# Optimization experiments

Measured on AMD Instinct MI355X. Metric: run time of the kernel, lower is better.

Reference implementation:

```python
import jax, jax.numpy as jnp
import numpy as np

B, K1, N, DIMS = 512, 11, 5, 784  # K1 = K+1 samples per class incl. query
H = 512  # model_size


def _lstm(x_seq, W, U, b):
    """Keras-style LSTM, return_sequences=True.
    x_seq: [B, T, I]; W: [I, 4H]; U: [H, 4H]; b: [4H]. Gate order i,f,g,o.
    """
    units = U.shape[0]
    bsz = x_seq.shape[0]
    # precompute input projections for all timesteps: [T, B, 4H]
    xw = jnp.einsum('bti,ih->tbh', x_seq, W) + b

    def step(carry, xw_t):
        h, c = carry
        z = xw_t + h @ U  # [B, 4H]
        i, f, g, o = jnp.split(z, 4, axis=-1)
        i = jax.nn.sigmoid(i)
        f = jax.nn.sigmoid(f)
        g = jnp.tanh(g)
        o = jax.nn.sigmoid(o)
        c = f * c + i * g
        h = o * jnp.tanh(c)
        return (h, c), h

    init = (jnp.zeros((bsz, units), x_seq.dtype), jnp.zeros((bsz, units), x_seq.dtype))
    _, hs = jax.lax.scan(step, init, xw)  # hs: [T, B, H]
    return jnp.transpose(hs, (1, 0, 2))  # [B, T, H]


def setup_inputs() -> dict:
    key = jax.random.key(0)
    ks = jax.random.split(key, 8)
    return {
        'input_images': jax.random.normal(ks[0], (B, K1, N, DIMS), jnp.float32),
        'input_labels': jax.random.uniform(ks[1], (B, K1, N, N), jnp.float32),
        'W1': jax.random.normal(ks[2], (N + DIMS, 4 * H), jnp.float32) * 0.02,
        'U1': jax.random.normal(ks[3], (H, 4 * H), jnp.float32) * 0.02,
        'b1': jnp.zeros((4 * H,), jnp.float32),
        'W2': jax.random.normal(ks[4], (H, 4 * N), jnp.float32) * 0.02,
        'U2': jax.random.normal(ks[5], (N, 4 * N), jnp.float32) * 0.02,
        'b2': jnp.zeros((4 * N,), jnp.float32),
    }


def reference(input_images, input_labels, W1, U1, b1, W2, U2, b2):
    K = K1 - 1
    support_imgs = input_images[:, :K]               # [B, K, N, D]
    query_imgs = input_images[:, -1].reshape(-1, 1, N, DIMS)  # [B, 1, N, D]
    support_lbls = input_labels[:, :K]               # [B, K, N, N]
    concat_support = jnp.concatenate([support_imgs, support_lbls], axis=-1)
    zero_lbls = jnp.zeros((B, 1, N, N), input_images.dtype)
    concat_query = jnp.concatenate([query_imgs, zero_lbls], axis=-1)
    seq = jnp.concatenate([concat_support, concat_query], axis=1)  # [B, K1, N, N+D]
    seq = seq.reshape(-1, N * K1, N + DIMS)          # [B, T, N+D], T = N*K1
    x = _lstm(seq, W1, U1, b1)                       # [B, T, H]
    out = _lstm(x, W2, U2, b2)                       # [B, T, N]
    return out.reshape(-1, K1, N, N)
```

## Files before the change

### kernel.cpp

```cpp
#include <hip/hip_runtime.h>

typedef __attribute__((ext_vector_type(8))) __bf16 bf16x8;
typedef __attribute__((ext_vector_type(8))) unsigned short ushort8;
typedef __attribute__((ext_vector_type(4))) float f32x4;
typedef __attribute__((ext_vector_type(2))) unsigned long long u64x2;

#define DEVINL __device__ __forceinline__
#define RLX __ATOMIC_RELAXED
#define AGT __HIP_MEMORY_SCOPE_AGENT

constexpr int B_C    = 512;
constexpr int DIMS_C = 784;
constexpr int T_C    = 55;
constexpr int I0_C   = 789;
constexpr int KP_C   = 800;
constexpr int H_C    = 512;
constexpr int G4_C   = 2048;
constexpr int M1_C   = 28160;

constexpr size_t OFF_A    = 0;
constexpr size_t SZ_A     = (size_t)M1_C * KP_C * 2;
constexpr size_t OFF_W1T  = OFF_A + SZ_A;
constexpr size_t SZ_W1T   = (size_t)G4_C * KP_C * 2;
constexpr size_t OFF_U1T  = OFF_W1T + SZ_W1T;
constexpr size_t SZ_U1T   = (size_t)G4_C * H_C * 2;
constexpr size_t OFF_XW1  = OFF_U1T + SZ_U1T;
constexpr size_t SZ_XW1   = (size_t)M1_C * G4_C * 2;
constexpr size_t OFF_H    = OFF_XW1 + SZ_XW1;
constexpr size_t SZ_H     = (size_t)2 * B_C * H_C * 2;
constexpr size_t OFF_XMID = OFF_H + SZ_H;
constexpr size_t SZ_XMID  = (size_t)M1_C * H_C * 4;
constexpr size_t OFF_XW2  = OFF_XMID + SZ_XMID;
constexpr size_t SZ_XW2   = (size_t)M1_C * 20 * 4;
constexpr size_t OFF_W2T  = OFF_XW2 + SZ_XW2;
constexpr size_t SZ_W2T   = (size_t)20 * H_C * 4;
constexpr size_t OFF_CNT  = OFF_W2T + SZ_W2T;

DEVINL unsigned short f2bf(float f) {
  unsigned u = __builtin_bit_cast(unsigned, f);
  u += 0x7fffu + ((u >> 16) & 1u);
  return (unsigned short)(u >> 16);
}
DEVINL float sigm(float x) {
  return __builtin_amdgcn_rcpf(1.f + __builtin_amdgcn_exp2f(-1.4426950408889634f * x));
}
DEVINL float tanh_(float x) {
  return 2.f * __builtin_amdgcn_rcpf(1.f + __builtin_amdgcn_exp2f(-2.8853900817779268f * x)) - 1.f;
}
DEVINL void gl_lds16(const void* g, void* l) {
  __builtin_amdgcn_global_load_lds((const __attribute__((address_space(1))) void*)g,
                                   (__attribute__((address_space(3))) void*)l, 16, 0, 0);
}
DEVINL void gl_lds16_coh(const void* g, void* l) {
  __builtin_amdgcn_global_load_lds((const __attribute__((address_space(1))) void*)g,
                                   (__attribute__((address_space(3))) void*)l, 16, 0, 17);
}


__global__ void pack_a(const float* __restrict__ img, const float* __restrict__ lbl,
                       unsigned short* __restrict__ A) {
  int gid = blockIdx.x * blockDim.x + threadIdx.x;
  constexpr int CPR = KP_C / 8;
  if (gid >= M1_C * CPR) return;
  int r  = gid / CPR;
  int cc = gid - r * CPR;
  int t = r >> 9, b = r & 511;
  int k1 = t / 5, n = t - k1 * 5;
  int c0 = cc * 8;
  ushort8 v;
  if (c0 + 8 <= DIMS_C) {
    const float* p = img + ((size_t)((b * 11 + k1) * 5 + n)) * DIMS_C + c0;
    f32x4 x0 = *(const f32x4*)(p);
    f32x4 x1 = *(const f32x4*)(p + 4);
#pragma unroll
    for (int j = 0; j < 4; ++j) { v[j] = f2bf(x0[j]); v[4 + j] = f2bf(x1[j]); }
  } else {
#pragma unroll
    for (int j = 0; j < 8; ++j) {
      int c = c0 + j;
      float x = 0.f;
      if (c < DIMS_C) x = img[((size_t)((b * 11 + k1) * 5 + n)) * DIMS_C + c];
      else if (c < I0_C && k1 < 10) x = lbl[((size_t)((b * 11 + k1) * 5 + n)) * 5 + (c - DIMS_C)];
      v[j] = f2bf(x);
    }
  }
  *(ushort8*)(A + (size_t)r * KP_C + c0) = v;
}

__global__ void pack_w1t(const float* __restrict__ W1, unsigned short* __restrict__ W1T) {
  int gid = blockIdx.x * blockDim.x + threadIdx.x;
  if (gid >= G4_C * KP_C) return;
  int col = gid / KP_C, k = gid - col * KP_C;
  float x = (k < I0_C) ? W1[(size_t)k * G4_C + col] : 0.f;
  W1T[(size_t)col * KP_C + k] = f2bf(x);
}

__global__ void pack_u1t(const float* __restrict__ U1, unsigned short* __restrict__ U1T) {
  int gid = blockIdx.x * blockDim.x + threadIdx.x;
  if (gid >= G4_C * H_C) return;
  int col = gid / H_C, k = gid - col * H_C;
  U1T[(size_t)col * H_C + k] = f2bf(U1[(size_t)k * G4_C + col]);
}

__global__ void pack_w2t(const float* __restrict__ W2, float* __restrict__ W2T) {
  int gid = blockIdx.x * blockDim.x + threadIdx.x;
  if (gid >= 20 * H_C) return;
  int col = gid / H_C, k = gid - col * H_C;
  W2T[(size_t)col * H_C + k] = W2[(size_t)k * 20 + col];
}

__launch_bounds__(256, 2)
__global__ void gemm1(const unsigned short* __restrict__ A,
                      const unsigned short* __restrict__ Bt,
                      const float* __restrict__ bias,
                      _Float16* __restrict__ C)
{
  __shared__ unsigned short sA[2][128 * 32];
  __shared__ unsigned short sB[2][128 * 32];
  const int tid = threadIdx.x;
  const int w = tid >> 6, l = tid & 63;
  const int lo = l & 15, hi = l >> 4;
  const int wm = w >> 1, wn = w & 1;
  const int bx = blockIdx.x;
  const int by = blockIdx.y;

  const unsigned short* aSrc[2];
  const unsigned short* bSrc[2];
#pragma unroll
  for (int q = 0; q < 2; ++q) {
    int row = w * 32 + q * 16 + (l >> 2);
    int ch = l & 3;
    int sw = (row >> 1) & 3;
    aSrc[q] = A  + (size_t)(by * 128 + row) * KP_C + (ch ^ sw) * 8;
    bSrc[q] = Bt + (size_t)(bx * 128 + row) * KP_C + (ch ^ sw) * 8;
  }
  int aOff[4], bOff[4];
#pragma unroll
  for (int i = 0; i < 4; ++i) {
    int rA = wm * 64 + i * 16 + lo;
    aOff[i] = rA * 32 + ((hi ^ ((rA >> 1) & 3)) * 8);
    int rB = wn * 64 + i * 16 + lo;
    bOff[i] = rB * 32 + ((hi ^ ((rB >> 1) & 3)) * 8);
  }

  f32x4 acc[4][4];
#pragma unroll
  for (int i = 0; i < 4; ++i)
#pragma unroll
    for (int j = 0; j < 4; ++j) acc[i][j] = (f32x4){0.f, 0.f, 0.f, 0.f};

#define G1_STAGE(buf, ks)                                                  \
  {                                                                        \
    _Pragma("unroll")                                                      \
    for (int q = 0; q < 2; ++q) {                                          \
      gl_lds16(aSrc[q] + (ks) * 32, &sA[buf][w * 1024 + q * 512]);         \
      gl_lds16(bSrc[q] + (ks) * 32, &sB[buf][w * 1024 + q * 512]);         \
    }                                                                      \
  }

  G1_STAGE(0, 0);
  asm volatile("s_waitcnt vmcnt(0)" ::: "memory");
  __syncthreads();

  int cur = 0;
#pragma unroll 1
  for (int ks = 0; ks < KP_C / 32; ++ks) {
    if (ks < KP_C / 32 - 1) G1_STAGE(cur ^ 1, ks + 1);
    bf16x8 af[4], bfr[4];
#pragma unroll
    for (int i = 0; i < 4; ++i) {
      af[i]  = *(const bf16x8*)(&sA[cur][0] + aOff[i]);
      bfr[i] = *(const bf16x8*)(&sB[cur][0] + bOff[i]);
    }
#pragma unroll
    for (int mi = 0; mi < 4; ++mi)
#pragma unroll
      for (int ni = 0; ni < 4; ++ni)
        acc[mi][ni] = __builtin_amdgcn_mfma_f32_16x16x32_bf16(af[mi], bfr[ni], acc[mi][ni], 0, 0, 0);
    asm volatile("s_waitcnt vmcnt(0)" ::: "memory");
    __syncthreads();
    cur ^= 1;
  }
#undef G1_STAGE

  const size_t crow0 = (size_t)by * 128 + wm * 64;
  const int ccol0 = bx * 128 + wn * 64;
#pragma unroll
  for (int ni = 0; ni < 4; ++ni) {
    int col = ccol0 + ni * 16 + lo;
    float bv = bias[col];
#pragma unroll
    for (int mi = 0; mi < 4; ++mi) {
#pragma unroll
      for (int j = 0; j < 4; ++j) {
        size_t row = crow0 + mi * 16 + hi * 4 + j;
        C[row * G4_C + col] = (_Float16)(acc[mi][ni][j] + bv);
      }
    }
  }
}

__launch_bounds__(256, 1)
__global__ void lstm1(const _Float16* __restrict__ xw,
                      const unsigned short* __restrict__ U1T,
                      unsigned short* __restrict__ hbuf,
                      float* __restrict__ xmid,
                      unsigned int* __restrict__ cnt)
{
  __shared__ unsigned short sH[32 * 512];
  __shared__ float sG[4 * 32 * 32];

  const int tid = threadIdx.x;
  const int g = tid >> 6;
  const int l = tid & 63;
  const int lo = l & 15, hi = l >> 4;
  const int bg = blockIdx.x >> 4;
  const int cg = blockIdx.x & 15;
  const int brow0 = bg * 32;
  const int ub = cg * 32;

  bf16x8 bu[2][16];
#pragma unroll
  for (int nf = 0; nf < 2; ++nf) {
    const unsigned short* src = U1T + ((size_t)(g * H_C + ub + nf * 16 + lo)) * H_C + hi * 8;
#pragma unroll
    for (int kk = 0; kk < 16; ++kk)
      bu[nf][kk] = *(const bf16x8*)(src + kk * 32);
  }

  const int s0 = lo & 7;
  const int aO0 = lo * 1024;
  const int aO1 = aO0 + 16 * 1024;

  const int half = l >> 5;
  const int u = l & 31;
  const int rbase = g * 8 + half * 4;
  const int uread = u ^ (((g * 2 + half) & 3) << 3);

  f32x4 c_st = (f32x4){0.f, 0.f, 0.f, 0.f};

  const _Float16* xb = xw + (size_t)(brow0 + rbase) * G4_C + ub + u;
  float xwv[4][4];
#pragma unroll
  for (int g2 = 0; g2 < 4; ++g2)
#pragma unroll
    for (int j = 0; j < 4; ++j)
      xwv[g2][j] = (float)xb[(size_t)j * G4_C + g2 * H_C];

#pragma unroll 1
  for (int t = 0; t < T_C; ++t) {
    f32x4 acc[2][2];
#pragma unroll
    for (int mf = 0; mf < 2; ++mf)
#pragma unroll
      for (int nf = 0; nf < 2; ++nf) acc[mf][nf] = (f32x4){0.f, 0.f, 0.f, 0.f};

    if (t > 0) {
      {
        const unsigned* fp = cnt + (size_t)(bg * 16 + (l & 15)) * 16;
        unsigned target = (unsigned)t;
        while (true) {
          unsigned v = __hip_atomic_load(fp, RLX, AGT);
          if (__all(v >= target)) break;
          __builtin_amdgcn_s_sleep(2);
        }
      }
      asm volatile("" ::: "memory");

      const unsigned short* hsrc = hbuf + (size_t)(t & 1) * (B_C * H_C);
#pragma unroll
      for (int p = 0; p < 8; ++p) {
        int row = g * 8 + p;
        gl_lds16_coh(hsrc + (size_t)(brow0 + row) * H_C + ((l ^ p) * 8),
                     sH + row * 512);
      }
      asm volatile("s_waitcnt vmcnt(0)" ::: "memory");
      __syncthreads();

#pragma unroll
      for (int kk = 0; kk < 16; ++kk) {
        int off = (((kk * 4 + hi) ^ s0) << 4);
        bf16x8 a0 = *(const bf16x8*)((const char*)sH + aO0 + off);
        bf16x8 a1 = *(const bf16x8*)((const char*)sH + aO1 + off);
        acc[0][0] = __builtin_amdgcn_mfma_f32_16x16x32_bf16(a0, bu[0][kk], acc[0][0], 0, 0, 0);
        acc[0][1] = __builtin_amdgcn_mfma_f32_16x16x32_bf16(a0, bu[1][kk], acc[0][1], 0, 0, 0);
        acc[1][0] = __builtin_amdgcn_mfma_f32_16x16x32_bf16(a1, bu[0][kk], acc[1][0], 0, 0, 0);
        acc[1][1] = __builtin_amdgcn_mfma_f32_16x16x32_bf16(a1, bu[1][kk], acc[1][1], 0, 0, 0);
      }
    }

#pragma unroll
    for (int mf = 0; mf < 2; ++mf)
#pragma unroll
      for (int nf = 0; nf < 2; ++nf)
#pragma unroll
        for (int j = 0; j < 4; ++j) {
          int row = mf * 16 + hi * 4 + j;
          sG[g * 1024 + row * 32 + ((nf * 16 + lo) ^ (hi << 3))] = acc[mf][nf][j];
        }
    __syncthreads();

    float hnew[4];
#pragma unroll
    for (int j = 0; j < 4; ++j) {
      int row = rbase + j;
      float zi = sG[0 * 1024 + row * 32 + uread] + xwv[0][j];
      float zf = sG[1 * 1024 + row * 32 + uread] + xwv[1][j];
      float zg = sG[2 * 1024 + row * 32 + uread] + xwv[2][j];
      float zo = sG[3 * 1024 + row * 32 + uread] + xwv[3][j];
      float iv = sigm(zi), fv = sigm(zf), gv = tanh_(zg), ov = sigm(zo);
      float cv = fv * c_st[j] + iv * gv;
      c_st[j] = cv;
      hnew[j] = ov * tanh_(cv);
    }

    if (t < T_C - 1) {
      unsigned short* hd = hbuf + (size_t)((t & 1) ^ 1) * (B_C * H_C);
#pragma unroll
      for (int j = 0; j < 4; ++j) {
        float other = __shfl_xor(hnew[j], 1);
        if ((u & 1) == 0) {
          unsigned val = (unsigned)f2bf(hnew[j]) | ((unsigned)f2bf(other) << 16);
          __hip_atomic_store((unsigned*)(hd + (size_t)(brow0 + rbase + j) * H_C + ub + u), val,
                             RLX, AGT);
        }
      }

      __syncthreads();
      if (tid == 0)
        __hip_atomic_store(&cnt[(size_t)(bg * 16 + cg) * 16], (unsigned)(t + 1), RLX, AGT);

#pragma unroll
      for (int j = 0; j < 4; ++j)
        __builtin_nontemporal_store(hnew[j],
            &xmid[((size_t)t * B_C + brow0 + rbase + j) * H_C + ub + u]);
      const _Float16* xp = xb + (size_t)(t + 1) * B_C * G4_C;
#pragma unroll
      for (int g2 = 0; g2 < 4; ++g2)
#pragma unroll
        for (int j = 0; j < 4; ++j)
          xwv[g2][j] = (float)xp[(size_t)j * G4_C + g2 * H_C];
    } else {
#pragma unroll
      for (int j = 0; j < 4; ++j)
        __builtin_nontemporal_store(hnew[j],
            &xmid[((size_t)t * B_C + brow0 + rbase + j) * H_C + ub + u]);
    }
  }
}

__global__ void gemm2(const float* __restrict__ X,
                      const float* __restrict__ W2T,
                      const float* __restrict__ b2,
                      float* __restrict__ XW2)
{
  int r = blockIdx.x * blockDim.x + threadIdx.x;
  if (r >= M1_C) return;
  float acc[20];
#pragma unroll
  for (int j = 0; j < 20; ++j) acc[j] = b2[j];
  const float* xr = X + (size_t)r * H_C;
  for (int k = 0; k < H_C; k += 4) {
    f32x4 xv = *(const f32x4*)(xr + k);
#pragma unroll
    for (int j = 0; j < 20; ++j) {
      f32x4 wv = *(const f32x4*)(W2T + (size_t)j * H_C + k);
      acc[j] += xv[0]*wv[0] + xv[1]*wv[1] + xv[2]*wv[2] + xv[3]*wv[3];
    }
  }
  float* op = XW2 + (size_t)r * 20;
#pragma unroll
  for (int j = 0; j < 20; ++j) op[j] = acc[j];
}

__global__ void lstm2(const float* __restrict__ XW2,
                      const float* __restrict__ U2,
                      float* __restrict__ out)
{
  int b = blockIdx.x * blockDim.x + threadIdx.x;
  if (b >= B_C) return;
  float u2[5][20];
#pragma unroll
  for (int k = 0; k < 5; ++k)
#pragma unroll
    for (int j = 0; j < 20; ++j) u2[k][j] = U2[k * 20 + j];
  float h[5] = {0, 0, 0, 0, 0}, c[5] = {0, 0, 0, 0, 0};
  for (int t = 0; t < T_C; ++t) {
    const float* xr = XW2 + ((size_t)t * B_C + b) * 20;
    float z[20];
#pragma unroll
    for (int j = 0; j < 20; ++j) z[j] = xr[j];
#pragma unroll
    for (int k = 0; k < 5; ++k) {
      float hk = h[k];
#pragma unroll
      for (int j = 0; j < 20; ++j) z[j] += hk * u2[k][j];
    }
#pragma unroll
    for (int n = 0; n < 5; ++n) {
      float iv = sigm(z[n]), fv = sigm(z[5 + n]), gv = tanh_(z[10 + n]), ov = sigm(z[15 + n]);
      c[n] = fv * c[n] + iv * gv;
      h[n] = ov * tanh_(c[n]);
    }
    int k1 = t / 5, nn = t - k1 * 5;
    float* op = out + (((size_t)b * 11 + k1) * 5 + nn) * 5;
#pragma unroll
    for (int j = 0; j < 5; ++j) op[j] = h[j];
  }
}

extern "C" void kernel_launch(void* const* d_in, const int* in_sizes, int n_in,
                              void* d_out, int out_size, void* d_ws, size_t ws_size,
                              hipStream_t stream) {
  (void)in_sizes; (void)n_in; (void)out_size; (void)ws_size;
  const float* img = (const float*)d_in[0];
  const float* lbl = (const float*)d_in[1];
  const float* W1  = (const float*)d_in[2];
  const float* U1  = (const float*)d_in[3];
  const float* b1  = (const float*)d_in[4];
  const float* W2  = (const float*)d_in[5];
  const float* U2  = (const float*)d_in[6];
  const float* b2  = (const float*)d_in[7];

  char* ws = (char*)d_ws;
  unsigned short* A    = (unsigned short*)(ws + OFF_A);
  unsigned short* W1T  = (unsigned short*)(ws + OFF_W1T);
  unsigned short* U1T  = (unsigned short*)(ws + OFF_U1T);
  _Float16*       XW1  = (_Float16*)      (ws + OFF_XW1);
  unsigned short* HB   = (unsigned short*)(ws + OFF_H);
  float*          XMID = (float*)         (ws + OFF_XMID);
  float*          XW2  = (float*)         (ws + OFF_XW2);
  float*          W2T  = (float*)         (ws + OFF_W2T);
  unsigned int*   CNT  = (unsigned int*)  (ws + OFF_CNT);

  hipMemsetAsync(CNT, 0, 256 * 64, stream);

  pack_a  <<<(M1_C * (KP_C / 8)) / 256, 256, 0, stream>>>(img, lbl, A);
  pack_w1t<<<(G4_C * KP_C) / 256,      256, 0, stream>>>(W1, W1T);
  pack_u1t<<<(G4_C * H_C) / 256,       256, 0, stream>>>(U1, U1T);
  pack_w2t<<<(20 * H_C + 255) / 256,   256, 0, stream>>>(W2, W2T);

  gemm1<<<dim3(G4_C / 128, M1_C / 128), 256, 0, stream>>>(A, W1T, b1, XW1);
  lstm1<<<256, 256, 0, stream>>>(XW1, U1T, HB, XMID, CNT);
  gemm2<<<(M1_C + 255) / 256, 256, 0, stream>>>(XMID, W2T, b2, XW2);
  lstm2<<<8, 64, 0, stream>>>(XW2, U2, (float*)d_out);
}
```

Baseline: 517.3 us.

## Remap LSTM gate columns to registers, drop LDS gate exchange, swizzle GEMM grid

```diff
diff --git a/kernel.cpp b/kernel.cpp
--- a/kernel.cpp
+++ b/kernel.cpp
@@ -121,8 +121,10 @@
   const int w = tid >> 6, l = tid & 63;
   const int lo = l & 15, hi = l >> 4;
   const int wm = w >> 1, wn = w & 1;
-  const int bx = blockIdx.x;
-  const int by = blockIdx.y;
+  const int id = blockIdx.x;
+  const int swz = (id & 7) * 440 + (id >> 3);
+  const int by = swz >> 4;
+  const int bx = swz & 15;
 
   const unsigned short* aSrc[2];
   const unsigned short* bSrc[2];
@@ -208,21 +210,23 @@
                       unsigned int* __restrict__ cnt)
 {
   __shared__ unsigned short sH[32 * 512];
-  __shared__ float sG[4 * 32 * 32];
 
   const int tid = threadIdx.x;
-  const int g = tid >> 6;
+  const int w = tid >> 6;
   const int l = tid & 63;
   const int lo = l & 15, hi = l >> 4;
+  const int q = lo & 7;
+  const int gsel = lo >> 3;
   const int bg = blockIdx.x >> 4;
   const int cg = blockIdx.x & 15;
   const int brow0 = bg * 32;
   const int ub = cg * 32;
+  const int unit = ub + w * 8 + q;
 
   bf16x8 bu[2][16];
 #pragma unroll
   for (int nf = 0; nf < 2; ++nf) {
-    const unsigned short* src = U1T + ((size_t)(g * H_C + ub + nf * 16 + lo)) * H_C + hi * 8;
+    const unsigned short* src = U1T + ((size_t)((nf * 2 + gsel) * H_C + unit)) * H_C + hi * 8;
 #pragma unroll
     for (int kk = 0; kk < 16; ++kk)
       bu[nf][kk] = *(const bf16x8*)(src + kk * 32);
@@ -232,20 +236,19 @@
   const int aO0 = lo * 1024;
   const int aO1 = aO0 + 16 * 1024;
 
-  const int half = l >> 5;
-  const int u = l & 31;
-  const int rbase = g * 8 + half * 4;
-  const int uread = u ^ (((g * 2 + half) & 3) << 3);
-
-  f32x4 c_st = (f32x4){0.f, 0.f, 0.f, 0.f};
-
-  const _Float16* xb = xw + (size_t)(brow0 + rbase) * G4_C + ub + u;
-  float xwv[4][4];
-#pragma unroll
-  for (int g2 = 0; g2 < 4; ++g2)
-#pragma unroll
-    for (int j = 0; j < 4; ++j)
-      xwv[g2][j] = (float)xb[(size_t)j * G4_C + g2 * H_C];
+  float c_st[8];
+#pragma unroll
+  for (int i = 0; i < 8; ++i) c_st[i] = 0.f;
+
+  const _Float16* xb = xw + (size_t)(brow0 + hi * 4) * G4_C + gsel * H_C + unit;
+  float xwv[2][2][4];
+#pragma unroll
+  for (int nf = 0; nf < 2; ++nf)
+#pragma unroll
+    for (int mf = 0; mf < 2; ++mf)
+#pragma unroll
+      for (int j = 0; j < 4; ++j)
+        xwv[nf][mf][j] = (float)xb[(size_t)(mf * 16 + j) * G4_C + nf * 1024];
 
 #pragma unroll 1
   for (int t = 0; t < T_C; ++t) {
@@ -262,7 +265,7 @@
         while (true) {
           unsigned v = __hip_atomic_load(fp, RLX, AGT);
           if (__all(v >= target)) break;
-          __builtin_amdgcn_s_sleep(2);
+          __builtin_amdgcn_s_sleep(1);
         }
       }
       asm volatile("" ::: "memory");
@@ -270,7 +273,7 @@
       const unsigned short* hsrc = hbuf + (size_t)(t & 1) * (B_C * H_C);
 #pragma unroll
       for (int p = 0; p < 8; ++p) {
-        int row = g * 8 + p;
+        int row = w * 8 + p;
         gl_lds16_coh(hsrc + (size_t)(brow0 + row) * H_C + ((l ^ p) * 8),
                      sH + row * 512);
       }
@@ -289,62 +292,72 @@
       }
     }
 
+    float hnew[8];
 #pragma unroll
     for (int mf = 0; mf < 2; ++mf)
 #pragma unroll
-      for (int nf = 0; nf < 2; ++nf)
-#pragma unroll
-        for (int j = 0; j < 4; ++j) {
-          int row = mf * 16 + hi * 4 + j;
-          sG[g * 1024 + row * 32 + ((nf * 16 + lo) ^ (hi << 3))] = acc[mf][nf][j];
-        }
-    __syncthreads();
-
-    float hnew[4];
-#pragma unroll
-    for (int j = 0; j < 4; ++j) {
-      int row = rbase + j;
-      float zi = sG[0 * 1024 + row * 32 + uread] + xwv[0][j];
-      float zf = sG[1 * 1024 + row * 32 + uread] + xwv[1][j];
-      float zg = sG[2 * 1024 + row * 32 + uread] + xwv[2][j];
-      float zo = sG[3 * 1024 + row * 32 + uread] + xwv[3][j];
-      float iv = sigm(zi), fv = sigm(zf), gv = tanh_(zg), ov = sigm(zo);
-      float cv = fv * c_st[j] + iv * gv;
-      c_st[j] = cv;
-      hnew[j] = ov * tanh_(cv);
-    }
+      for (int j = 0; j < 4; ++j) {
+        float za = acc[mf][0][j] + xwv[0][mf][j];
+        float zb = acc[mf][1][j] + xwv[1][mf][j];
+        float zap = __shfl_xor(za, 8);
+        float zbp = __shfl_xor(zb, 8);
+        float zi = gsel ? zap : za;
+        float zf = gsel ? za : zap;
+        float zg = gsel ? zbp : zb;
+        float zo = gsel ? zb : zbp;
+        float iv = sigm(zi), fv = sigm(zf), gv = tanh_(zg), ov = sigm(zo);
+        int ci = mf * 4 + j;
+        float cv = fv * c_st[ci] + iv * gv;
+        c_st[ci] = cv;
+        hnew[ci] = ov * tanh_(cv);
+      }
 
     if (t < T_C - 1) {
       unsigned short* hd = hbuf + (size_t)((t & 1) ^ 1) * (B_C * H_C);
 #pragma unroll
-      for (int j = 0; j < 4; ++j) {
-        float other = __shfl_xor(hnew[j], 1);
-        if ((u & 1) == 0) {
-          unsigned val = (unsigned)f2bf(hnew[j]) | ((unsigned)f2bf(other) << 16);
-          __hip_atomic_store((unsigned*)(hd + (size_t)(brow0 + rbase + j) * H_C + ub + u), val,
-                             RLX, AGT);
+      for (int mf = 0; mf < 2; ++mf)
+#pragma unroll
+        for (int j = 0; j < 4; ++j) {
+          int ci = mf * 4 + j;
+          float other = __shfl_xor(hnew[ci], 1);
+          if (lo < 8 && (q & 1) == 0) {
+            int row = mf * 16 + hi * 4 + j;
+            unsigned val = (unsigned)f2bf(hnew[ci]) | ((unsigned)f2bf(other) << 16);
+            __hip_atomic_store((unsigned*)(hd + (size_t)(brow0 + row) * H_C + unit), val,
+                               RLX, AGT);
+          }
         }
-      }
-
+
+#pragma unroll
+      for (int mf = 0; mf < 2; ++mf)
+#pragma unroll
+        for (int j = 0; j < 4; ++j)
+          if (lo < 8) {
+            int row = mf * 16 + hi * 4 + j;
+            xmid[((size_t)t * B_C + brow0 + row) * H_C + unit] = hnew[mf * 4 + j];
+          }
+      const _Float16* xp = xb + (size_t)(t + 1) * B_C * G4_C;
+#pragma unroll
+      for (int nf = 0; nf < 2; ++nf)
+#pragma unroll
+        for (int mf = 0; mf < 2; ++mf)
+#pragma unroll
+          for (int j = 0; j < 4; ++j)
+            xwv[nf][mf][j] = (float)xp[(size_t)(mf * 16 + j) * G4_C + nf * 1024];
+
+      asm volatile("s_waitcnt vmcnt(0)" ::: "memory");
       __syncthreads();
       if (tid == 0)
         __hip_atomic_store(&cnt[(size_t)(bg * 16 + cg) * 16], (unsigned)(t + 1), RLX, AGT);
-
-#pragma unroll
-      for (int j = 0; j < 4; ++j)
-        __builtin_nontemporal_store(hnew[j],
-            &xmid[((size_t)t * B_C + brow0 + rbase + j) * H_C + ub + u]);
-      const _Float16* xp = xb + (size_t)(t + 1) * B_C * G4_C;
-#pragma unroll
-      for (int g2 = 0; g2 < 4; ++g2)
+    } else {
+#pragma unroll
+      for (int mf = 0; mf < 2; ++mf)
 #pragma unroll
         for (int j = 0; j < 4; ++j)
-          xwv[g2][j] = (float)xp[(size_t)j * G4_C + g2 * H_C];
-    } else {
-#pragma unroll
-      for (int j = 0; j < 4; ++j)
-        __builtin_nontemporal_store(hnew[j],
-            &xmid[((size_t)t * B_C + brow0 + rbase + j) * H_C + ub + u]);
+          if (lo < 8) {
+            int row = mf * 16 + hi * 4 + j;
+            xmid[((size_t)t * B_C + brow0 + row) * H_C + unit] = hnew[mf * 4 + j];
+          }
     }
   }
 }
@@ -440,7 +453,7 @@
   pack_u1t<<<(G4_C * H_C) / 256,       256, 0, stream>>>(U1, U1T);
   pack_w2t<<<(20 * H_C + 255) / 256,   256, 0, stream>>>(W2, W2T);
 
-  gemm1<<<dim3(G4_C / 128, M1_C / 128), 256, 0, stream>>>(A, W1T, b1, XW1);
+  gemm1<<<3520, 256, 0, stream>>>(A, W1T, b1, XW1);
   lstm1<<<256, 256, 0, stream>>>(XW1, U1T, HB, XMID, CNT);
   gemm2<<<(M1_C + 255) / 256, 256, 0, stream>>>(XMID, W2T, b2, XW2);
   lstm2<<<8, 64, 0, stream>>>(XW2, U2, (float*)d_out);
```

Result: slower. 557.1 us (+7.7%).

## Halve LSTM1 batch rows per block, double grid, and swizzle GEMM1 block order

Applied to the files above, without the earlier changes.

```diff
diff --git a/kernel.cpp b/kernel.cpp
--- a/kernel.cpp
+++ b/kernel.cpp
@@ -121,8 +121,10 @@
   const int w = tid >> 6, l = tid & 63;
   const int lo = l & 15, hi = l >> 4;
   const int wm = w >> 1, wn = w & 1;
-  const int bx = blockIdx.x;
-  const int by = blockIdx.y;
+  const int id = blockIdx.x;
+  const int swz = (id & 7) * 440 + (id >> 3);
+  const int by = swz >> 4;
+  const int bx = swz & 15;
 
   const unsigned short* aSrc[2];
   const unsigned short* bSrc[2];
@@ -200,15 +202,15 @@
   }
 }
 
-__launch_bounds__(256, 1)
+__launch_bounds__(256, 2)
 __global__ void lstm1(const _Float16* __restrict__ xw,
                       const unsigned short* __restrict__ U1T,
                       unsigned short* __restrict__ hbuf,
                       float* __restrict__ xmid,
                       unsigned int* __restrict__ cnt)
 {
-  __shared__ unsigned short sH[32 * 512];
-  __shared__ float sG[4 * 32 * 32];
+  __shared__ unsigned short sH[16 * 512];
+  __shared__ float sG[4 * 16 * 32];
 
   const int tid = threadIdx.x;
   const int g = tid >> 6;
@@ -216,7 +218,7 @@
   const int lo = l & 15, hi = l >> 4;
   const int bg = blockIdx.x >> 4;
   const int cg = blockIdx.x & 15;
-  const int brow0 = bg * 32;
+  const int brow0 = bg * 16;
   const int ub = cg * 32;
 
   bf16x8 bu[2][16];
@@ -230,30 +232,27 @@
 
   const int s0 = lo & 7;
   const int aO0 = lo * 1024;
-  const int aO1 = aO0 + 16 * 1024;
 
   const int half = l >> 5;
   const int u = l & 31;
-  const int rbase = g * 8 + half * 4;
-  const int uread = u ^ (((g * 2 + half) & 3) << 3);
-
-  f32x4 c_st = (f32x4){0.f, 0.f, 0.f, 0.f};
+  const int rbase = g * 4 + half * 2;
+  const int uread = u ^ (g << 3);
+
+  float c_st[2] = {0.f, 0.f};
 
   const _Float16* xb = xw + (size_t)(brow0 + rbase) * G4_C + ub + u;
-  float xwv[4][4];
+  float xwv[4][2];
 #pragma unroll
   for (int g2 = 0; g2 < 4; ++g2)
 #pragma unroll
-    for (int j = 0; j < 4; ++j)
+    for (int j = 0; j < 2; ++j)
       xwv[g2][j] = (float)xb[(size_t)j * G4_C + g2 * H_C];
 
 #pragma unroll 1
   for (int t = 0; t < T_C; ++t) {
-    f32x4 acc[2][2];
-#pragma unroll
-    for (int mf = 0; mf < 2; ++mf)
-#pragma unroll
-      for (int nf = 0; nf < 2; ++nf) acc[mf][nf] = (f32x4){0.f, 0.f, 0.f, 0.f};
+    f32x4 acc[2];
+    acc[0] = (f32x4){0.f, 0.f, 0.f, 0.f};
+    acc[1] = (f32x4){0.f, 0.f, 0.f, 0.f};
 
     if (t > 0) {
       {
@@ -262,16 +261,16 @@
         while (true) {
           unsigned v = __hip_atomic_load(fp, RLX, AGT);
           if (__all(v >= target)) break;
-          __builtin_amdgcn_s_sleep(2);
+          __builtin_amdgcn_s_sleep(1);
         }
       }
       asm volatile("" ::: "memory");
 
       const unsigned short* hsrc = hbuf + (size_t)(t & 1) * (B_C * H_C);
 #pragma unroll
-      for (int p = 0; p < 8; ++p) {
-        int row = g * 8 + p;
-        gl_lds16_coh(hsrc + (size_t)(brow0 + row) * H_C + ((l ^ p) * 8),
+      for (int p = 0; p < 4; ++p) {
+        int row = g * 4 + p;
+        gl_lds16_coh(hsrc + (size_t)(brow0 + row) * H_C + ((l ^ (row & 7)) * 8),
                      sH + row * 512);
       }
       asm volatile("s_waitcnt vmcnt(0)" ::: "memory");
@@ -281,33 +280,28 @@
       for (int kk = 0; kk < 16; ++kk) {
         int off = (((kk * 4 + hi) ^ s0) << 4);
         bf16x8 a0 = *(const bf16x8*)((const char*)sH + aO0 + off);
-        bf16x8 a1 = *(const bf16x8*)((const char*)sH + aO1 + off);
-        acc[0][0] = __builtin_amdgcn_mfma_f32_16x16x32_bf16(a0, bu[0][kk], acc[0][0], 0, 0, 0);
-        acc[0][1] = __builtin_amdgcn_mfma_f32_16x16x32_bf16(a0, bu[1][kk], acc[0][1], 0, 0, 0);
-        acc[1][0] = __builtin_amdgcn_mfma_f32_16x16x32_bf16(a1, bu[0][kk], acc[1][0], 0, 0, 0);
-        acc[1][1] = __builtin_amdgcn_mfma_f32_16x16x32_bf16(a1, bu[1][kk], acc[1][1], 0, 0, 0);
-      }
-    }
-
-#pragma unroll
-    for (int mf = 0; mf < 2; ++mf)
-#pragma unroll
-      for (int nf = 0; nf < 2; ++nf)
-#pragma unroll
-        for (int j = 0; j < 4; ++j) {
-          int row = mf * 16 + hi * 4 + j;
-          sG[g * 1024 + row * 32 + ((nf * 16 + lo) ^ (hi << 3))] = acc[mf][nf][j];
-        }
+        acc[0] = __builtin_amdgcn_mfma_f32_16x16x32_bf16(a0, bu[0][kk], acc[0], 0, 0, 0);
+        acc[1] = __builtin_amdgcn_mfma_f32_16x16x32_bf16(a0, bu[1][kk], acc[1], 0, 0, 0);
+      }
+    }
+
+#pragma unroll
+    for (int nf = 0; nf < 2; ++nf)
+#pragma unroll
+      for (int j = 0; j < 4; ++j) {
+        int row = hi * 4 + j;
+        sG[g * 512 + row * 32 + ((nf * 16 + lo) ^ (hi << 3))] = acc[nf][j];
+      }
     __syncthreads();
 
-    float hnew[4];
-#pragma unroll
-    for (int j = 0; j < 4; ++j) {
-      int row = rbase + j;
-      float zi = sG[0 * 1024 + row * 32 + uread] + xwv[0][j];
-      float zf = sG[1 * 1024 + row * 32 + uread] + xwv[1][j];
-      float zg = sG[2 * 1024 + row * 32 + uread] + xwv[2][j];
-      float zo = sG[3 * 1024 + row * 32 + uread] + xwv[3][j];
+    float hnew[2];
+#pragma unroll
+    for (int j = 0; j < 2; ++j) {
+      int r = rbase + j;
+      float zi = sG[0 * 512 + r * 32 + uread] + xwv[0][j];
+      float zf = sG[1 * 512 + r * 32 + uread] + xwv[1][j];
+      float zg = sG[2 * 512 + r * 32 + uread] + xwv[2][j];
+      float zo = sG[3 * 512 + r * 32 + uread] + xwv[3][j];
       float iv = sigm(zi), fv = sigm(zf), gv = tanh_(zg), ov = sigm(zo);
       float cv = fv * c_st[j] + iv * gv;
       c_st[j] = cv;
@@ -317,7 +311,7 @@
     if (t < T_C - 1) {
       unsigned short* hd = hbuf + (size_t)((t & 1) ^ 1) * (B_C * H_C);
 #pragma unroll
-      for (int j = 0; j < 4; ++j) {
+      for (int j = 0; j < 2; ++j) {
         float other = __shfl_xor(hnew[j], 1);
         if ((u & 1) == 0) {
           unsigned val = (unsigned)f2bf(hnew[j]) | ((unsigned)f2bf(other) << 16);
@@ -331,18 +325,18 @@
         __hip_atomic_store(&cnt[(size_t)(bg * 16 + cg) * 16], (unsigned)(t + 1), RLX, AGT);
 
 #pragma unroll
-      for (int j = 0; j < 4; ++j)
+      for (int j = 0; j < 2; ++j)
         __builtin_nontemporal_store(hnew[j],
             &xmid[((size_t)t * B_C + brow0 + rbase + j) * H_C + ub + u]);
       const _Float16* xp = xb + (size_t)(t + 1) * B_C * G4_C;
 #pragma unroll
       for (int g2 = 0; g2 < 4; ++g2)
 #pragma unroll
-        for (int j = 0; j < 4; ++j)
+        for (int j = 0; j < 2; ++j)
           xwv[g2][j] = (float)xp[(size_t)j * G4_C + g2 * H_C];
     } else {
 #pragma unroll
-      for (int j = 0; j < 4; ++j)
+      for (int j = 0; j < 2; ++j)
         __builtin_nontemporal_store(hnew[j],
             &xmid[((size_t)t * B_C + brow0 + rbase + j) * H_C + ub + u]);
     }
@@ -433,15 +427,15 @@
   float*          W2T  = (float*)         (ws + OFF_W2T);
   unsigned int*   CNT  = (unsigned int*)  (ws + OFF_CNT);
 
-  hipMemsetAsync(CNT, 0, 256 * 64, stream);
+  hipMemsetAsync(CNT, 0, 512 * 64, stream);
 
   pack_a  <<<(M1_C * (KP_C / 8)) / 256, 256, 0, stream>>>(img, lbl, A);
   pack_w1t<<<(G4_C * KP_C) / 256,      256, 0, stream>>>(W1, W1T);
   pack_u1t<<<(G4_C * H_C) / 256,       256, 0, stream>>>(U1, U1T);
   pack_w2t<<<(20 * H_C + 255) / 256,   256, 0, stream>>>(W2, W2T);
 
-  gemm1<<<dim3(G4_C / 128, M1_C / 128), 256, 0, stream>>>(A, W1T, b1, XW1);
-  lstm1<<<256, 256, 0, stream>>>(XW1, U1T, HB, XMID, CNT);
+  gemm1<<<3520, 256, 0, stream>>>(A, W1T, b1, XW1);
+  lstm1<<<512, 256, 0, stream>>>(XW1, U1T, HB, XMID, CNT);
   gemm2<<<(M1_C + 255) / 256, 256, 0, stream>>>(XMID, W2T, b2, XW2);
   lstm2<<<8, 64, 0, stream>>>(XW2, U2, (float*)d_out);
 }
```

After: 458.2 us. 11.4% less time.
